# Kernel tuning notes

Measured on AMD Instinct MI355X. Metric: run time of the kernel, lower is better.

Reference implementation:

```python
import jax, jax.numpy as jnp
import numpy as np

H = 4096          # hidden_size
NH = 32           # num_attention_heads
NKV = 2           # multi_query_group_num (kv heads)
HD = 128          # kv_channels / head_dim
RD = 64           # rotary_dim = head_dim * rotary_percent(0.5)
T = 2048          # total tokens (single prefill sequence)
EPS = 1e-5        # layernorm_epsilon
ROPE_BASE = 10000.0


def setup_inputs() -> dict:
    key = jax.random.key(0)
    k0, k1, k2, k3 = jax.random.split(key, 4)
    qkv_out = (NH + 2 * NKV) * HD  # 4608
    return {
        "positions": jnp.arange(T, dtype=jnp.int32),
        "hidden_states": jax.random.normal(k0, (T, H), jnp.float32),
        "w_qkv": jax.random.normal(k1, (qkv_out, H), jnp.float32) * 0.02,
        "b_qkv": jax.random.normal(k2, (qkv_out,), jnp.float32) * 0.02,
        "w_dense": jax.random.normal(k3, (H, NH * HD), jnp.float32) * 0.02,
        "q_ln_w": jnp.ones((HD,), jnp.float32),
        "k_ln_w": jnp.ones((HD,), jnp.float32),
    }


def _rmsnorm(x, w):
    # per-head RMSNorm over head_dim
    return x * jax.lax.rsqrt(jnp.mean(x * x, axis=-1, keepdims=True) + EPS) * w


def _rope(x, positions):
    # partial rotary (first RD dims), interleaved GPT-J style (is_neox_style=False)
    inv_freq = 1.0 / (ROPE_BASE ** (jnp.arange(0, RD, 2, dtype=jnp.float32) / RD))
    ang = positions.astype(jnp.float32)[:, None] * inv_freq      # [T, RD//2]
    cos = jnp.cos(ang)[:, None, :]                               # [T, 1, RD//2]
    sin = jnp.sin(ang)[:, None, :]
    x_rot, x_pass = x[..., :RD], x[..., RD:]
    x1 = x_rot[..., 0::2]
    x2 = x_rot[..., 1::2]
    r1 = x1 * cos - x2 * sin
    r2 = x2 * cos + x1 * sin
    x_rot = jnp.stack([r1, r2], axis=-1).reshape(x.shape[:-1] + (RD,))
    return jnp.concatenate([x_rot, x_pass], axis=-1)


def reference(positions, hidden_states, w_qkv, b_qkv, w_dense, q_ln_w, k_ln_w):
    qkv = hidden_states @ w_qkv.T + b_qkv                        # [T, 4608]
    q_size, kv_size = NH * HD, NKV * HD
    q = qkv[:, :q_size].reshape(T, NH, HD)
    k = qkv[:, q_size:q_size + kv_size].reshape(T, NKV, HD)
    v = qkv[:, q_size + kv_size:].reshape(T, NKV, HD)
    # optional qk layernorm (RMSNorm since config.rmsnorm)
    q = _rmsnorm(q, q_ln_w)
    k = _rmsnorm(k, k_ln_w)
    # rotary embedding
    q = _rope(q, positions)
    k = _rope(k, positions)
    # GQA: expand kv heads to query heads
    group = NH // NKV
    k_exp = jnp.repeat(k, group, axis=1)                         # [T, NH, HD]
    v_exp = jnp.repeat(v, group, axis=1)
    scale = HD ** -0.5
    scores = jnp.einsum("thd,shd->hts", q, k_exp) * scale        # [NH, T, T]
    causal = jnp.tril(jnp.ones((T, T), dtype=bool))
    scores = jnp.where(causal[None, :, :], scores, jnp.finfo(scores.dtype).min)
    attn = jax.nn.softmax(scores, axis=-1)
    out = jnp.einsum("hts,shd->thd", attn, v_exp).reshape(T, NH * HD)
    return out @ w_dense.T                                       # [T, H]
```

## Files before the change

kernel.cpp:

```cpp
#include <hip/hip_runtime.h>
#include <cstdint>
#include <cstddef>

typedef short short4v __attribute__((ext_vector_type(4)));
typedef short short8v __attribute__((ext_vector_type(8)));
typedef float f32x4   __attribute__((ext_vector_type(4)));

#define T_LEN  2048
#define HDIM   4096
#define NHEADS 32
#define HEADD  128
#define QKVN   4608

static __device__ __forceinline__ short f2bf(float f) {
  __bf16 h = (__bf16)f;
  return __builtin_bit_cast(short, h);
}
static __device__ __forceinline__ float bf2f(short u) {
  return __builtin_bit_cast(float, ((unsigned int)(unsigned short)u) << 16);
}

static __device__ __forceinline__ void gload_lds16(const void* g, void* l) {
  __builtin_amdgcn_global_load_lds((const __attribute__((address_space(1))) void*)g,
                                   (__attribute__((address_space(3))) void*)l,
                                   16, 0, 0);
}

__global__ void cast_pair(const float* __restrict__ a, short* __restrict__ oa, int na4,
                          const float* __restrict__ b, short* __restrict__ ob, int nb4) {
  int idx = blockIdx.x * blockDim.x + threadIdx.x;
  int stride = gridDim.x * blockDim.x;
  const int ntot = na4 + nb4;
  for (int i = idx; i < ntot; i += stride) {
    const float4* src = (i < na4) ? ((const float4*)a + i) : ((const float4*)b + (i - na4));
    short4v* dst      = (i < na4) ? ((short4v*)oa + i)     : ((short4v*)ob + (i - na4));
    float4 v = *src;
    short4v o;
    o[0] = f2bf(v.x); o[1] = f2bf(v.y); o[2] = f2bf(v.z); o[3] = f2bf(v.w);
    *dst = o;
  }
}

template <int OUT_BF16>
__global__ __launch_bounds__(256, 2) void gemm_bt(
    const short* __restrict__ A,
    const short* __restrict__ B,
    const float* __restrict__ bias,
    void* __restrict__ Cout,
    int M, int N, int K)
{
  __shared__ short sA[2][128 * 32];
  __shared__ short sB[2][128 * 32];
  const int tid  = threadIdx.x;
  const int lane = tid & 63;
  const int wv   = tid >> 6;
  const int wr   = wv >> 1;
  const int wc   = wv & 1;

  const int nwg  = gridDim.x * gridDim.y;
  int wgid = blockIdx.y * gridDim.x + blockIdx.x;
  wgid = (wgid & 7) * (nwg >> 3) + (wgid >> 3);
  const int bn0 = (wgid / gridDim.y) * 128;
  const int bm0 = (wgid % gridDim.y) * 128;

  const int row0 = tid >> 2;
  const int kc0  = (tid & 3) * 8;
  const int row1 = row0 + 64;
  const short* gA0 = A + (size_t)(bm0 + row0) * K + kc0;
  const short* gA1 = A + (size_t)(bm0 + row1) * K + kc0;
  const short* gB0 = B + (size_t)(bn0 + row0) * K + kc0;
  const short* gB1 = B + (size_t)(bn0 + row1) * K + kc0;

  const int fr = lane & 15;
  const int fk = (lane >> 4) * 8;

  auto STAGE = [&](int b, int kt) {
    short* lA = &sA[b][0] + wv * 64 * 8;
    short* lB = &sB[b][0] + wv * 64 * 8;
    gload_lds16(gA0 + kt, lA);
    gload_lds16(gA1 + kt, lA + 256 * 8);
    gload_lds16(gB0 + kt, lB);
    gload_lds16(gB1 + kt, lB + 256 * 8);
  };

  f32x4 zero = {0.f, 0.f, 0.f, 0.f};
  f32x4 acc[4][4];
#pragma unroll
  for (int m = 0; m < 4; m++)
#pragma unroll
    for (int n = 0; n < 4; n++) acc[m][n] = zero;

  int cur = 0;
  STAGE(0, 0);
  __syncthreads();

  for (int kt = 0; kt < K; kt += 32) {
    if (kt + 32 < K) STAGE(cur ^ 1, kt + 32);
    const short* aB = &sA[cur][0];
    const short* bB = &sB[cur][0];
    short8v af[4], bfr[4];
#pragma unroll
    for (int m = 0; m < 4; m++)
      af[m] = *(const short8v*)(aB + (wr * 64 + m * 16 + fr) * 32 + fk);
#pragma unroll
    for (int n = 0; n < 4; n++)
      bfr[n] = *(const short8v*)(bB + (wc * 64 + n * 16 + fr) * 32 + fk);
#pragma unroll
    for (int m = 0; m < 4; m++)
#pragma unroll
      for (int n = 0; n < 4; n++)
        acc[m][n] = __builtin_amdgcn_mfma_f32_16x16x32_bf16(af[m], bfr[n], acc[m][n], 0, 0, 0);
    __syncthreads();
    cur ^= 1;
  }

  const int rg = (lane >> 4) * 4;
#pragma unroll
  for (int m = 0; m < 4; m++) {
#pragma unroll
    for (int n = 0; n < 4; n++) {
      const int gcol = bn0 + wc * 64 + n * 16 + fr;
      const float bv = bias ? bias[gcol] : 0.0f;
#pragma unroll
      for (int j = 0; j < 4; j++) {
        const int grow = bm0 + wr * 64 + m * 16 + rg + j;
        const float v = acc[m][n][j] + bv;
        if (OUT_BF16)
          ((short*)Cout)[(size_t)grow * N + gcol] = f2bf(v);
        else
          ((float*)Cout)[(size_t)grow * N + gcol] = v;
      }
    }
  }
}

__global__ __launch_bounds__(256) void qkv_post_kernel(
    const short* __restrict__ qkvb,
    const int*   __restrict__ positions,
    const float* __restrict__ q_ln,
    const float* __restrict__ k_ln,
    short* __restrict__ Qb,
    short* __restrict__ Kb,
    short* __restrict__ Vt)
{
  const int t = blockIdx.x;
  const int h = blockIdx.y * 4 + (threadIdx.x >> 6);
  const int lane = threadIdx.x & 63;
  const unsigned int pk =
      ((const unsigned int*)(qkvb + (size_t)t * QKVN + h * HEADD))[lane];
  float x = bf2f((short)(pk & 0xffffu));
  float y = bf2f((short)(pk >> 16));

  if (h >= 34) {
    const int hv = h - 34;
    short* dst = Vt + ((size_t)hv * HEADD + 2 * lane) * T_LEN + t;
    dst[0]     = f2bf(x);
    dst[T_LEN] = f2bf(y);
    return;
  }

  float ss = x * x + y * y;
#pragma unroll
  for (int d = 32; d > 0; d >>= 1) ss += __shfl_xor(ss, d);
  const float r = rsqrtf(ss * (1.0f / 128.0f) + 1e-5f);
  const float* lnw = (h < 32) ? q_ln : k_ln;
  x = x * r * lnw[2 * lane];
  y = y * r * lnw[2 * lane + 1];

  if (lane < 32) {
    const float pos = (float)positions[t];
    const float ang = pos * powf(10000.0f, -(float)lane * (1.0f / 32.0f));
    const float c = cosf(ang), s = sinf(ang);
    const float r1 = x * c - y * s;
    const float r2 = y * c + x * s;
    x = r1; y = r2;
  }

  short* dst = (h < 32) ? (Qb + ((size_t)h * T_LEN + t) * HEADD + 2 * lane)
                        : (Kb + ((size_t)(h - 32) * T_LEN + t) * HEADD + 2 * lane);
  dst[0] = f2bf(x);
  dst[1] = f2bf(y);
}

__global__ __launch_bounds__(256, 2) void attn_kernel(
    const short* __restrict__ Qb,
    const short* __restrict__ Kb,
    const short* __restrict__ Vt,
    short* __restrict__ attn_out,
    const float* __restrict__ wd_src,
    short* __restrict__ wd_dst)
{
  __shared__ short Ks[2][64 * 128];
  __shared__ short Vs[2][128 * 64];
  __shared__ short pbuf[4][32 * 64];
  const int tid  = threadIdx.x;

  if (blockIdx.z == 1) {
    const int bid = blockIdx.y * gridDim.x + blockIdx.x;
    const int stride = gridDim.x * gridDim.y * 256;
    const float4* s4 = (const float4*)wd_src;
    short4v* d4 = (short4v*)wd_dst;
    for (int i = bid * 256 + tid; i < (HDIM * HDIM) / 4; i += stride) {
      float4 v = s4[i];
      short4v o;
      o[0] = f2bf(v.x); o[1] = f2bf(v.y); o[2] = f2bf(v.z); o[3] = f2bf(v.w);
      d4[i] = o;
    }
    return;
  }

  const int blk  = gridDim.x - 1 - blockIdx.x;
  const int h    = blockIdx.y;
  const int hkv  = h >> 4;
  const int lane = tid & 63;
  const int wv   = tid >> 6;
  const int B0   = blk * 128;
  const int qrow0 = B0 + wv * 32;
  const int fr = lane & 15;
  const int fk = (lane >> 4) * 8;
  const int fkb = (lane >> 4) << 4;
  const int rg = (lane >> 4) * 4;
  const int swz = (fr & 7) << 4;

  const short* Kh = Kb + (size_t)hkv * T_LEN * HEADD;
  const short* Vh = Vt + (size_t)hkv * HEADD * T_LEN;

  short8v qf[2][4];
#pragma unroll
  for (int g = 0; g < 2; g++) {
    const short* Qrow = Qb + ((size_t)h * T_LEN + qrow0 + g * 16 + fr) * HEADD + fk;
#pragma unroll
    for (int d0 = 0; d0 < 4; d0++) qf[g][d0] = *(const short8v*)(Qrow + d0 * 32);
  }

  float mrow[2][4], lrow[2][4];
#pragma unroll
  for (int g = 0; g < 2; g++)
#pragma unroll
    for (int j = 0; j < 4; j++) { mrow[g][j] = -1e30f; lrow[g][j] = 0.f; }
  f32x4 zero = {0.f, 0.f, 0.f, 0.f};
  f32x4 o[2][8];
#pragma unroll
  for (int g = 0; g < 2; g++)
#pragma unroll
    for (int d = 0; d < 8; d++) o[g][d] = zero;

  char* pb = (char*)&pbuf[wv][0];
  const float scale = 0.08838834764831845f;
  const int nt = 2 * blk + 2;

  auto STAGE = [&](int b, int t) {
    const int s0 = t * 64;
#pragma unroll
    for (int i = 0; i < 4; i++) {
      const int c    = i * 256 + tid;
      const int row  = c >> 4;
      const int colb = (c & 15) << 4;
      const int scol = (colb ^ ((row & 7) << 4)) >> 1;
      gload_lds16(Kh + (size_t)(s0 + row) * HEADD + scol,
                  (char*)&Ks[b][0] + (size_t)(i * 256 + wv * 64) * 16);
    }
#pragma unroll
    for (int i = 0; i < 4; i++) {
      const int c    = i * 256 + tid;
      const int row  = c >> 3;
      const int colb = (c & 7) << 4;
      const int scol = (colb ^ ((row & 7) << 4)) >> 1;
      gload_lds16(Vh + (size_t)row * T_LEN + s0 + scol,
                  (char*)&Vs[b][0] + (size_t)(i * 256 + wv * 64) * 16);
    }
  };

  int cur = 0;
  STAGE(0, 0);
  __syncthreads();

  for (int t = 0; t < nt; ++t) {
    if (t + 1 < nt) STAGE(cur ^ 1, t + 1);
    const int s0 = t * 64;
    const char* KsB = (const char*)&Ks[cur][0];
    const char* VsB = (const char*)&Vs[cur][0];

    float scv[2][4][4];
    __builtin_amdgcn_s_setprio(1);
#pragma unroll
    for (int sub = 0; sub < 4; sub++) {
      const char* Kbase = KsB + (sub * 16 + fr) * 256;
      f32x4 a0 = zero, a1 = zero;
#pragma unroll
      for (int d0 = 0; d0 < 4; d0++) {
        short8v kf = *(const short8v*)(Kbase + ((d0 * 64 + fkb) ^ swz));
        a0 = __builtin_amdgcn_mfma_f32_16x16x32_bf16(qf[0][d0], kf, a0, 0, 0, 0);
        a1 = __builtin_amdgcn_mfma_f32_16x16x32_bf16(qf[1][d0], kf, a1, 0, 0, 0);
      }
#pragma unroll
      for (int j = 0; j < 4; j++) {
        scv[0][sub][j] = a0[j] * scale;
        scv[1][sub][j] = a1[j] * scale;
      }
    }
    __builtin_amdgcn_s_setprio(0);
    if (t >= nt - 2) {
#pragma unroll
      for (int g = 0; g < 2; g++)
#pragma unroll
        for (int sub = 0; sub < 4; sub++) {
          const int colp = s0 + sub * 16 + fr;
#pragma unroll
          for (int j = 0; j < 4; j++)
            if (colp > qrow0 + g * 16 + rg + j) scv[g][sub][j] = -1e30f;
        }
    }
    float pmax[2][4];
#pragma unroll
    for (int g = 0; g < 2; g++)
#pragma unroll
      for (int j = 0; j < 4; j++)
        pmax[g][j] = fmaxf(fmaxf(scv[g][0][j], scv[g][1][j]),
                           fmaxf(scv[g][2][j], scv[g][3][j]));
    float growth = -1e30f;
#pragma unroll
    for (int g = 0; g < 2; g++)
#pragma unroll
      for (int j = 0; j < 4; j++) growth = fmaxf(growth, pmax[g][j] - mrow[g][j]);
    if (!__all(growth <= 8.0f)) {
#pragma unroll
      for (int g = 0; g < 2; g++)
#pragma unroll
        for (int j = 0; j < 4; j++) {
          float mx = pmax[g][j];
#pragma unroll
          for (int d = 1; d < 16; d <<= 1) mx = fmaxf(mx, __shfl_xor(mx, d));
          const float mn = fmaxf(mrow[g][j], mx);
          const float c  = __expf(mrow[g][j] - mn);
          mrow[g][j] = mn;
          lrow[g][j] *= c;
#pragma unroll
          for (int df = 0; df < 8; df++) o[g][df][j] *= c;
        }
    }
#pragma unroll
    for (int g = 0; g < 2; g++)
#pragma unroll
      for (int j = 0; j < 4; j++) {
        const int prow = g * 16 + rg + j;
        char* prb = pb + prow * 128;
        const int rswz = ((rg + j) & 7) << 4;
        float ps = 0.f;
#pragma unroll
        for (int sub = 0; sub < 4; sub++) {
          const float p = __expf(scv[g][sub][j] - mrow[g][j]);
          ps += p;
          *(short*)(prb + ((((sub * 16 + fr) << 1)) ^ rswz)) = f2bf(p);
        }
        lrow[g][j] += ps;
      }
    asm volatile("" ::: "memory");
    short8v pf[2][2];
#pragma unroll
    for (int g = 0; g < 2; g++)
#pragma unroll
      for (int ks = 0; ks < 2; ks++)
        pf[g][ks] = *(const short8v*)(pb + (g * 16 + fr) * 128 + ((ks * 64 + fkb) ^ swz));
    __builtin_amdgcn_s_setprio(1);
#pragma unroll
    for (int df = 0; df < 8; df++) {
      const char* Vbase = VsB + (df * 16 + fr) * 128;
      short8v vf0 = *(const short8v*)(Vbase + ((0 + fkb) ^ swz));
      short8v vf1 = *(const short8v*)(Vbase + ((64 + fkb) ^ swz));
      o[0][df] = __builtin_amdgcn_mfma_f32_16x16x32_bf16(pf[0][0], vf0, o[0][df], 0, 0, 0);
      o[0][df] = __builtin_amdgcn_mfma_f32_16x16x32_bf16(pf[0][1], vf1, o[0][df], 0, 0, 0);
      o[1][df] = __builtin_amdgcn_mfma_f32_16x16x32_bf16(pf[1][0], vf0, o[1][df], 0, 0, 0);
      o[1][df] = __builtin_amdgcn_mfma_f32_16x16x32_bf16(pf[1][1], vf1, o[1][df], 0, 0, 0);
    }
    __builtin_amdgcn_s_setprio(0);
    __syncthreads();
    cur ^= 1;
  }

#pragma unroll
  for (int g = 0; g < 2; g++)
#pragma unroll
    for (int j = 0; j < 4; j++) {
#pragma unroll
      for (int d = 1; d < 16; d <<= 1) lrow[g][j] += __shfl_xor(lrow[g][j], d);
    }
#pragma unroll
  for (int g = 0; g < 2; g++)
#pragma unroll
    for (int df = 0; df < 8; df++)
#pragma unroll
      for (int j = 0; j < 4; j++) {
        const float v = o[g][df][j] / lrow[g][j];
        attn_out[(size_t)(qrow0 + g * 16 + rg + j) * HDIM + h * HEADD + df * 16 + fr] = f2bf(v);
      }
}

extern "C" void kernel_launch(void* const* d_in, const int* in_sizes, int n_in,
                              void* d_out, int out_size, void* d_ws, size_t ws_size,
                              hipStream_t stream) {
  (void)out_size; (void)ws_size;
  int ip = 0, ih = 1, iwq = 2, ib = 3, iwd = 4, il0 = 5, il1 = 6;
  if (n_in == 7) {
    int p = -1, hh = -1, wq = -1, b = -1, wd = -1, l0 = -1, l1 = -1, ok = 1;
    for (int i = 0; i < 7; i++) {
      switch (in_sizes[i]) {
        case 2048:     p  = i; break;
        case 8388608:  hh = i; break;
        case 18874368: wq = i; break;
        case 4608:     b  = i; break;
        case 16777216: wd = i; break;
        case 128:      if (l0 < 0) l0 = i; else l1 = i; break;
        default:       ok = 0; break;
      }
    }
    if (ok && p >= 0 && hh >= 0 && wq >= 0 && b >= 0 && wd >= 0 && l0 >= 0 && l1 >= 0) {
      ip = p; ih = hh; iwq = wq; ib = b; iwd = wd; il0 = l0; il1 = l1;
    }
  }

  const int*   positions = (const int*)d_in[ip];
  const float* hidden    = (const float*)d_in[ih];
  const float* w_qkv     = (const float*)d_in[iwq];
  const float* b_qkv     = (const float*)d_in[ib];
  const float* w_dense   = (const float*)d_in[iwd];
  const float* q_ln      = (const float*)d_in[il0];
  const float* k_ln      = (const float*)d_in[il1];

  char* ws = (char*)d_ws;
  short* Ahs   = (short*)(ws + 0);
  short* Qb    = (short*)(ws + 0);
  short* Wqkv  = (short*)(ws + (size_t)16777216);
  short* Kb    = (short*)(ws + (size_t)16777216);
  short* Vt    = (short*)(ws + (size_t)17825792);
  short* Wd    = (short*)(ws + (size_t)18874368);
  short* qkvb  = (short*)(ws + (size_t)54525952);
  short* attnb = (short*)(ws + (size_t)54525952);

  cast_pair<<<dim3(3072), dim3(256), 0, stream>>>(
      hidden, Ahs, (T_LEN * HDIM) / 4, w_qkv, Wqkv, (QKVN * HDIM) / 4);
  gemm_bt<1><<<dim3(QKVN / 128, T_LEN / 128), dim3(256), 0, stream>>>(
      Ahs, Wqkv, b_qkv, (void*)qkvb, T_LEN, QKVN, HDIM);
  qkv_post_kernel<<<dim3(T_LEN, 9), dim3(256), 0, stream>>>(
      qkvb, positions, q_ln, k_ln, Qb, Kb, Vt);
  attn_kernel<<<dim3(16, NHEADS, 2), dim3(256), 0, stream>>>(
      Qb, Kb, Vt, attnb, w_dense, Wd);
  gemm_bt<0><<<dim3(HDIM / 128, T_LEN / 128), dim3(256), 0, stream>>>(
      attnb, Wd, nullptr, d_out, T_LEN, HDIM, HDIM);
}
```

Before: 351.8 us.

## Split-K both GEMMs into two halves with bf16 partials and reduction kernels

New measurement: 381.4 us. 8.4% more time.

```diff
diff --git a/kernel.cpp b/kernel.cpp
--- a/kernel.cpp
+++ b/kernel.cpp
@@ -41,12 +41,10 @@
   }
 }
 
-template <int OUT_BF16>
-__global__ __launch_bounds__(256, 2) void gemm_bt(
+__global__ __launch_bounds__(256, 2) void gemm_splitk(
     const short* __restrict__ A,
     const short* __restrict__ B,
-    const float* __restrict__ bias,
-    void* __restrict__ Cout,
+    short* __restrict__ Cp,
     int M, int N, int K)
 {
   __shared__ short sA[2][128 * 32];
@@ -56,6 +54,8 @@
   const int wv   = tid >> 6;
   const int wr   = wv >> 1;
   const int wc   = wv & 1;
+  const int z    = blockIdx.z;
+  const int Khalf = K >> 1;
 
   const int nwg  = gridDim.x * gridDim.y;
   int wgid = blockIdx.y * gridDim.x + blockIdx.x;
@@ -66,10 +66,10 @@
   const int row0 = tid >> 2;
   const int kc0  = (tid & 3) * 8;
   const int row1 = row0 + 64;
-  const short* gA0 = A + (size_t)(bm0 + row0) * K + kc0;
-  const short* gA1 = A + (size_t)(bm0 + row1) * K + kc0;
-  const short* gB0 = B + (size_t)(bn0 + row0) * K + kc0;
-  const short* gB1 = B + (size_t)(bn0 + row1) * K + kc0;
+  const short* gA0 = A + (size_t)(bm0 + row0) * K + z * Khalf + kc0;
+  const short* gA1 = A + (size_t)(bm0 + row1) * K + z * Khalf + kc0;
+  const short* gB0 = B + (size_t)(bn0 + row0) * K + z * Khalf + kc0;
+  const short* gB1 = B + (size_t)(bn0 + row1) * K + z * Khalf + kc0;
 
   const int fr = lane & 15;
   const int fk = (lane >> 4) * 8;
@@ -94,8 +94,8 @@
   STAGE(0, 0);
   __syncthreads();
 
-  for (int kt = 0; kt < K; kt += 32) {
-    if (kt + 32 < K) STAGE(cur ^ 1, kt + 32);
+  for (int kt = 0; kt < Khalf; kt += 32) {
+    if (kt + 32 < Khalf) STAGE(cur ^ 1, kt + 32);
     const short* aB = &sA[cur][0];
     const short* bB = &sB[cur][0];
     short8v af[4], bfr[4];
@@ -114,24 +114,59 @@
     cur ^= 1;
   }
 
+  short* Cout = Cp + (size_t)z * M * N;
   const int rg = (lane >> 4) * 4;
 #pragma unroll
   for (int m = 0; m < 4; m++) {
 #pragma unroll
     for (int n = 0; n < 4; n++) {
       const int gcol = bn0 + wc * 64 + n * 16 + fr;
-      const float bv = bias ? bias[gcol] : 0.0f;
 #pragma unroll
       for (int j = 0; j < 4; j++) {
         const int grow = bm0 + wr * 64 + m * 16 + rg + j;
-        const float v = acc[m][n][j] + bv;
-        if (OUT_BF16)
-          ((short*)Cout)[(size_t)grow * N + gcol] = f2bf(v);
-        else
-          ((float*)Cout)[(size_t)grow * N + gcol] = v;
-      }
-    }
-  }
+        Cout[(size_t)grow * N + gcol] = f2bf(acc[m][n][j]);
+      }
+    }
+  }
+}
+
+__global__ __launch_bounds__(256) void reduce_bias_bf16(
+    const short* __restrict__ Cp, const float* __restrict__ bias,
+    short* __restrict__ out, size_t pstride, int ncol8) {
+  const int i = blockIdx.x * blockDim.x + threadIdx.x;
+  short8v a = ((const short8v*)Cp)[i];
+  short8v b = ((const short8v*)(Cp + pstride))[i];
+  const int col0 = (i % ncol8) * 8;
+  const float4 b0 = *(const float4*)(bias + col0);
+  const float4 b1 = *(const float4*)(bias + col0 + 4);
+  short8v o;
+  o[0] = f2bf(bf2f(a[0]) + bf2f(b[0]) + b0.x);
+  o[1] = f2bf(bf2f(a[1]) + bf2f(b[1]) + b0.y);
+  o[2] = f2bf(bf2f(a[2]) + bf2f(b[2]) + b0.z);
+  o[3] = f2bf(bf2f(a[3]) + bf2f(b[3]) + b0.w);
+  o[4] = f2bf(bf2f(a[4]) + bf2f(b[4]) + b1.x);
+  o[5] = f2bf(bf2f(a[5]) + bf2f(b[5]) + b1.y);
+  o[6] = f2bf(bf2f(a[6]) + bf2f(b[6]) + b1.z);
+  o[7] = f2bf(bf2f(a[7]) + bf2f(b[7]) + b1.w);
+  ((short8v*)out)[i] = o;
+}
+
+__global__ __launch_bounds__(256) void reduce_f32(
+    const short* __restrict__ Cp, float* __restrict__ out, size_t pstride) {
+  const int i = blockIdx.x * blockDim.x + threadIdx.x;
+  short8v a = ((const short8v*)Cp)[i];
+  short8v b = ((const short8v*)(Cp + pstride))[i];
+  float4 o0, o1;
+  o0.x = bf2f(a[0]) + bf2f(b[0]);
+  o0.y = bf2f(a[1]) + bf2f(b[1]);
+  o0.z = bf2f(a[2]) + bf2f(b[2]);
+  o0.w = bf2f(a[3]) + bf2f(b[3]);
+  o1.x = bf2f(a[4]) + bf2f(b[4]);
+  o1.y = bf2f(a[5]) + bf2f(b[5]);
+  o1.z = bf2f(a[6]) + bf2f(b[6]);
+  o1.w = bf2f(a[7]) + bf2f(b[7]);
+  ((float4*)out)[2 * i]     = o0;
+  ((float4*)out)[2 * i + 1] = o1;
 }
 
 __global__ __launch_bounds__(256) void qkv_post_kernel(
@@ -429,22 +464,28 @@
 
   char* ws = (char*)d_ws;
   short* Ahs   = (short*)(ws + 0);
-  short* Qb    = (short*)(ws + 0);
   short* Wqkv  = (short*)(ws + (size_t)16777216);
-  short* Kb    = (short*)(ws + (size_t)16777216);
-  short* Vt    = (short*)(ws + (size_t)17825792);
-  short* Wd    = (short*)(ws + (size_t)18874368);
-  short* qkvb  = (short*)(ws + (size_t)54525952);
-  short* attnb = (short*)(ws + (size_t)54525952);
+  short* Cp1   = (short*)(ws + (size_t)54525952);
+  short* qkvb  = (short*)(ws + 0);
+  short* Qb    = (short*)(ws + (size_t)18874368);
+  short* Kb    = (short*)(ws + (size_t)35651584);
+  short* Vt    = (short*)(ws + (size_t)36700160);
+  short* Wd    = (short*)(ws + (size_t)37748736);
+  short* attnb = (short*)(ws + (size_t)71303168);
+  short* Cp2   = (short*)(ws + 0);
 
   cast_pair<<<dim3(3072), dim3(256), 0, stream>>>(
       hidden, Ahs, (T_LEN * HDIM) / 4, w_qkv, Wqkv, (QKVN * HDIM) / 4);
-  gemm_bt<1><<<dim3(QKVN / 128, T_LEN / 128), dim3(256), 0, stream>>>(
-      Ahs, Wqkv, b_qkv, (void*)qkvb, T_LEN, QKVN, HDIM);
+  gemm_splitk<<<dim3(QKVN / 128, T_LEN / 128, 2), dim3(256), 0, stream>>>(
+      Ahs, Wqkv, Cp1, T_LEN, QKVN, HDIM);
+  reduce_bias_bf16<<<dim3((T_LEN * QKVN) / 8 / 256), dim3(256), 0, stream>>>(
+      Cp1, b_qkv, qkvb, (size_t)T_LEN * QKVN, QKVN / 8);
   qkv_post_kernel<<<dim3(T_LEN, 9), dim3(256), 0, stream>>>(
       qkvb, positions, q_ln, k_ln, Qb, Kb, Vt);
   attn_kernel<<<dim3(16, NHEADS, 2), dim3(256), 0, stream>>>(
       Qb, Kb, Vt, attnb, w_dense, Wd);
-  gemm_bt<0><<<dim3(HDIM / 128, T_LEN / 128), dim3(256), 0, stream>>>(
-      attnb, Wd, nullptr, d_out, T_LEN, HDIM, HDIM);
-}
+  gemm_splitk<<<dim3(HDIM / 128, T_LEN / 128, 2), dim3(256), 0, stream>>>(
+      attnb, Wd, Cp2, T_LEN, HDIM, HDIM);
+  reduce_f32<<<dim3((T_LEN * HDIM) / 8 / 256), dim3(256), 0, stream>>>(
+      Cp2, (float*)d_out, (size_t)T_LEN * HDIM);
+}
```
